# Kernel tuning notes

Measured on AMD Instinct MI355X. Metric: run time of the kernel, lower is better.

The kernel has to match this reference:

```python
import jax, jax.numpy as jnp
import numpy as np

B, C, H, W = 4, 128, 64, 64


def setup_inputs() -> dict:
    key = jax.random.key(0)
    k1, k2 = jax.random.split(key)
    x = jax.random.normal(k1, (B, C, H, W), dtype=jnp.float32)
    # 1x1 conv kv_mapper: weight [C_out, C_in], bias [C_out]; C_out == C_in == C
    W_kv = jax.random.normal(k2, (C, C), dtype=jnp.float32) * (1.0 / np.sqrt(C))
    b_kv = jnp.zeros((C,), dtype=jnp.float32)
    return {"x": x, "W_kv": W_kv, "b_kv": b_kv}


def reference(x, W_kv, b_kv):
    b, c, h, w = x.shape
    # kv_mapper: 1x1 conv  -> v: [b, c, h, w]
    v = jnp.einsum('bchw,oc->bohw', x, W_kv) + b_kv[None, :, None, None]
    # rearrange 'b c h w -> b (h w) c'
    L = h * w
    values = v.reshape(b, c, L).transpose(0, 2, 1)    # keys == values
    queries = x.reshape(b, c, L).transpose(0, 2, 1)
    # scaled dot-product attention, full [b, L, L] scores
    scores = jnp.einsum('blc,btc->blt', queries, values) / jnp.sqrt(jnp.asarray(c, x.dtype))
    attn = jax.nn.softmax(scores, axis=-1)
    out = jnp.einsum('blt,btv->blv', attn, values)    # [b, L, c]
    # rearrange 'b (h w) c -> b c h w'
    return out.transpose(0, 2, 1).reshape(b, c, h, w)
```

## Files before the change

kernel.cpp:

```cpp
#include <hip/hip_runtime.h>

#define LQ 4096
#define CH 128
#define NB 4
#define QSCALE 0.12753139626233174f
#define MAXCH 8
#define TILE_HW 8192

typedef __attribute__((ext_vector_type(8))) unsigned short ushort8;
typedef __attribute__((ext_vector_type(4))) unsigned short ushort4v;
typedef __attribute__((ext_vector_type(4))) unsigned int uint32x4;
typedef __attribute__((ext_vector_type(8))) __bf16 bf16x8;
typedef __attribute__((ext_vector_type(4))) float f32x4;

__device__ inline unsigned short f2bf(float f) {
    unsigned int u = __builtin_bit_cast(unsigned int, f);
    u += 0x7fffu + ((u >> 16) & 1u);
    return (unsigned short)(u >> 16);
}
__device__ inline float bf2f(unsigned short h) {
    unsigned int u = (unsigned int)h << 16;
    return __builtin_bit_cast(float, u);
}
__device__ inline unsigned int bfpack2(float a, float b) {
    unsigned int ua = __builtin_bit_cast(unsigned int, a) + 0x8000u;
    unsigned int ub = __builtin_bit_cast(unsigned int, b) + 0x8000u;
    return (ua >> 16) | (ub & 0xffff0000u);
}
__device__ inline void gload_lds16(const unsigned short* g, unsigned short* l) {
    __builtin_amdgcn_global_load_lds(
        (const __attribute__((address_space(1))) unsigned int*)(g),
        (__attribute__((address_space(3))) unsigned int*)(l), 16, 0, 0);
}

__global__ __launch_bounds__(256) void prep_kernel(
    const float* __restrict__ x, const float* __restrict__ Wkv,
    const float* __restrict__ bkv,
    unsigned short* __restrict__ Vt2, unsigned short* __restrict__ Vc2)
{
    __shared__ __align__(16) unsigned short xs[64 * 136];
    __shared__ __align__(16) unsigned short vs[128 * 72];
    const int tid = threadIdx.x;
    const int lane = tid & 63;
    const int wave = tid >> 6;
    const int quad = lane >> 4, l16 = lane & 15;
    const int b = blockIdx.x & 3;
    const int T = blockIdx.x >> 2;
    const int l0 = T << 6;

    {
        const f32x4* xg4 = (const f32x4*)(x + (size_t)b * CH * LQ + l0);
        #pragma unroll
        for (int i = 0; i < 8; ++i) {
            int idx = i * 256 + tid;
            int c = idx >> 4, l4 = idx & 15;
            f32x4 v = xg4[c * (LQ / 4) + l4];
            #pragma unroll
            for (int m = 0; m < 4; ++m) xs[(l4 * 4 + m) * 136 + c] = f2bf(v[m]);
        }
    }
    __syncthreads();

    const int wo = wave * 32;
    f32x4 acc[2][4];
    #pragma unroll
    for (int ot = 0; ot < 2; ++ot)
        #pragma unroll
        for (int lt = 0; lt < 4; ++lt) acc[ot][lt] = f32x4{0.f, 0.f, 0.f, 0.f};

    #pragma unroll
    for (int kc = 0; kc < 4; ++kc) {
        bf16x8 af[2];
        #pragma unroll
        for (int ot = 0; ot < 2; ++ot) {
            const float* wrow = Wkv + (size_t)(wo + ot * 16 + l16) * CH + kc * 32 + quad * 8;
            f32x4 w0 = *(const f32x4*)(wrow);
            f32x4 w1 = *(const f32x4*)(wrow + 4);
            ushort8 a;
            #pragma unroll
            for (int j = 0; j < 4; ++j) { a[j] = f2bf(w0[j]); a[j + 4] = f2bf(w1[j]); }
            af[ot] = __builtin_bit_cast(bf16x8, a);
        }
        #pragma unroll
        for (int lt = 0; lt < 4; ++lt) {
            bf16x8 bf = __builtin_bit_cast(bf16x8,
                *(const ushort8*)(xs + (lt * 16 + l16) * 136 + kc * 32 + quad * 8));
            #pragma unroll
            for (int ot = 0; ot < 2; ++ot)
                acc[ot][lt] = __builtin_amdgcn_mfma_f32_16x16x32_bf16(af[ot], bf, acc[ot][lt], 0, 0, 0);
        }
    }
    #pragma unroll
    for (int ot = 0; ot < 2; ++ot) {
        float bias[4];
        #pragma unroll
        for (int r = 0; r < 4; ++r) bias[r] = bkv[wo + ot * 16 + quad * 4 + r];
        #pragma unroll
        for (int lt = 0; lt < 4; ++lt)
            #pragma unroll
            for (int r = 0; r < 4; ++r)
                vs[(wo + ot * 16 + quad * 4 + r) * 72 + lt * 16 + l16] =
                    f2bf(acc[ot][lt][r] + bias[r]);
    }
    __syncthreads();
    const size_t tbase = ((size_t)b * 64 + T) * TILE_HW;
    #pragma unroll
    for (int i = 0; i < 4; ++i) {
        const int ci = i * 256 + tid;
        const int g = ci >> 6, ls = ci & 63;
        const int nt = g >> 2, kc = g & 3, qs = ls >> 4, l16s = ls & 15;
        ushort8 v;
        #pragma unroll
        for (int j = 0; j < 8; ++j) v[j] = vs[(kc * 32 + qs * 8 + j) * 72 + nt * 16 + l16s];
        *(ushort8*)(Vt2 + tbase + (size_t)ci * 8) = v;
    }
    #pragma unroll
    for (int i = 0; i < 4; ++i) {
        const int ci = i * 256 + tid;
        const int g = ci >> 6, ls = ci & 63;
        const int a = g >> 3, nc = g & 7, qs = ls >> 4, l16s = ls & 15;
        const int base = (nc * 16 + l16s) * 72 + a * 32 + qs * 4;
        ushort4v lo4 = *(const ushort4v*)(vs + base);
        ushort4v hi4 = *(const ushort4v*)(vs + base + 16);
        ushort8 v;
        #pragma unroll
        for (int j = 0; j < 4; ++j) { v[j] = lo4[j]; v[j + 4] = hi4[j]; }
        *(ushort8*)(Vc2 + tbase + (size_t)ci * 8) = v;
    }
}

__global__ __launch_bounds__(256, 2) void attn_kernel(
    const float* __restrict__ x, const unsigned short* __restrict__ Vt2,
    const unsigned short* __restrict__ Vc2,
    unsigned short* __restrict__ Opart, float* __restrict__ Lsum, int titers)
{
    __shared__ __align__(16) unsigned short bufA[TILE_HW];
    __shared__ __align__(16) unsigned short bufB[TILE_HW];
    const int tid = threadIdx.x;
    const int wave = tid >> 6, lane = tid & 63;
    const int quad = lane >> 4, l16 = lane & 15;
    const int b = blockIdx.x & 3;
    const int rest = blockIdx.x >> 2;
    const int qtile = rest & 31;
    const int chunk = rest >> 5;
    const int q0w = (qtile << 7) + (wave << 5);
    const int Tbase = chunk * titers;

    const unsigned short* vtb = Vt2 + (size_t)b * 64 * TILE_HW;
    const unsigned short* vcb = Vc2 + (size_t)b * 64 * TILE_HW;

    auto issueA = [&](int T) {
        const unsigned short* sa = vtb + (size_t)T * TILE_HW + lane * 8;
        #pragma unroll
        for (int g = 0; g < 4; ++g) {
            const int go = (wave * 4 + g) * 512;
            gload_lds16(sa + go, &bufA[go]);
        }
    };
    auto issueB = [&](int T) {
        const unsigned short* sb = vcb + (size_t)T * TILE_HW + lane * 8;
        #pragma unroll
        for (int g = 0; g < 4; ++g) {
            const int go = (wave * 4 + g) * 512;
            gload_lds16(sb + go, &bufB[go]);
        }
    };
    issueA(Tbase);

    bf16x8 qf[2][4];
    #pragma unroll
    for (int mt = 0; mt < 2; ++mt)
        #pragma unroll
        for (int kc = 0; kc < 4; ++kc) {
            ushort8 v;
            #pragma unroll
            for (int j = 0; j < 8; ++j) {
                int c = kc * 32 + quad * 8 + j;
                v[j] = f2bf(x[((size_t)b * CH + c) * LQ + q0w + mt * 16 + l16] * QSCALE);
            }
            qf[mt][kc] = __builtin_bit_cast(bf16x8, v);
        }

    f32x4 oacc[2][8];
    #pragma unroll
    for (int mt = 0; mt < 2; ++mt)
        #pragma unroll
        for (int i = 0; i < 8; ++i) oacc[mt][i] = f32x4{0.f, 0.f, 0.f, 0.f};
    float lsum[2] = {0.f, 0.f};

    for (int it = 0; it < titers; ++it) {
        asm volatile("s_waitcnt vmcnt(0)" ::: "memory");
        __builtin_amdgcn_s_barrier();
        issueB(Tbase + it);

        uint32x4 pk[2][2];

        #pragma unroll
        for (int nt = 0; nt < 4; ++nt) {
            const int aIdx = nt >> 1, h = nt & 1;
            bf16x8 vA[4];
            #pragma unroll
            for (int kc = 0; kc < 4; ++kc)
                vA[kc] = __builtin_bit_cast(bf16x8,
                    *(const ushort8*)(bufA + (nt * 4 + kc) * 512 + lane * 8));
            f32x4 s[2];
            __builtin_amdgcn_s_setprio(1);
            #pragma unroll
            for (int mt = 0; mt < 2; ++mt) {
                s[mt] = f32x4{0.f, 0.f, 0.f, 0.f};
                #pragma unroll
                for (int kc = 0; kc < 4; ++kc)
                    s[mt] = __builtin_amdgcn_mfma_f32_16x16x32_bf16(vA[kc], qf[mt][kc], s[mt], 0, 0, 0);
            }
            __builtin_amdgcn_s_setprio(0);
            #pragma unroll
            for (int mt = 0; mt < 2; ++mt) {
                float p0 = __builtin_amdgcn_exp2f(s[mt][0]);
                float p1 = __builtin_amdgcn_exp2f(s[mt][1]);
                float p2 = __builtin_amdgcn_exp2f(s[mt][2]);
                float p3 = __builtin_amdgcn_exp2f(s[mt][3]);
                lsum[mt] += (p0 + p1) + (p2 + p3);
                pk[mt][aIdx][h * 2 + 0] = bfpack2(p0, p1);
                pk[mt][aIdx][h * 2 + 1] = bfpack2(p2, p3);
            }
        }

        asm volatile("s_waitcnt vmcnt(0) lgkmcnt(0)" ::: "memory");
        __builtin_amdgcn_s_barrier();
        if (it + 1 < titers) issueA(Tbase + it + 1);

        __builtin_amdgcn_s_setprio(1);
        #pragma unroll
        for (int a = 0; a < 2; ++a) {
            bf16x8 pa0 = __builtin_bit_cast(bf16x8, pk[0][a]);
            bf16x8 pa1 = __builtin_bit_cast(bf16x8, pk[1][a]);
            #pragma unroll
            for (int nc = 0; nc < 8; ++nc) {
                bf16x8 vB = __builtin_bit_cast(bf16x8,
                    *(const ushort8*)(bufB + (a * 8 + nc) * 512 + lane * 8));
                oacc[0][nc] = __builtin_amdgcn_mfma_f32_16x16x32_bf16(pa0, vB, oacc[0][nc], 0, 0, 0);
                oacc[1][nc] = __builtin_amdgcn_mfma_f32_16x16x32_bf16(pa1, vB, oacc[1][nc], 0, 0, 0);
            }
        }
        __builtin_amdgcn_s_setprio(0);
    }
    const size_t pbase = ((size_t)(chunk * NB + b) * LQ);
    #pragma unroll
    for (int mt = 0; mt < 2; ++mt) {
        float v = lsum[mt];
        v += __shfl_xor(v, 16);
        v += __shfl_xor(v, 32);
        if (lane < 16) Lsum[pbase + q0w + mt * 16 + lane] = v;
    }
    #pragma unroll
    for (int mt = 0; mt < 2; ++mt)
        #pragma unroll
        for (int r = 0; r < 4; ++r) {
            const int q = q0w + mt * 16 + quad * 4 + r;
            unsigned short* orow = Opart + (pbase + q) * CH + l16;
            #pragma unroll
            for (int nc = 0; nc < 8; ++nc) orow[nc * 16] = f2bf(oacc[mt][nc][r]);
        }
}

__global__ __launch_bounds__(256) void combine_kernel(
    const unsigned short* __restrict__ Opart, const float* __restrict__ Lsum,
    float* __restrict__ out, int nchunk)
{
    __shared__ __align__(16) float ls[32 * 132];
    __shared__ float linv[32];
    const int tid = threadIdx.x;
    const int b = blockIdx.x & 3;
    const int q0 = (blockIdx.x >> 2) << 5;

    if (tid < 32) {
        float s = 0.f;
        for (int ch = 0; ch < nchunk; ++ch) s += Lsum[(size_t)(ch * NB + b) * LQ + q0 + tid];
        linv[tid] = 1.0f / s;
    }
    __syncthreads();
    {
        const int c8 = (tid & 15) * 8, qg = tid >> 4;
        #pragma unroll
        for (int i = 0; i < 2; ++i) {
            const int q = qg * 2 + i;
            float s[8];
            #pragma unroll
            for (int k = 0; k < 8; ++k) s[k] = 0.f;
            for (int ch = 0; ch < nchunk; ++ch) {
                ushort8 p = *(const ushort8*)(Opart +
                    ((size_t)(ch * NB + b) * LQ + q0 + q) * CH + c8);
                #pragma unroll
                for (int k = 0; k < 8; ++k) s[k] += bf2f(p[k]);
            }
            const float li = linv[q];
            f32x4 o0, o1;
            #pragma unroll
            for (int k = 0; k < 4; ++k) { o0[k] = s[k] * li; o1[k] = s[k + 4] * li; }
            *(f32x4*)(ls + q * 132 + c8) = o0;
            *(f32x4*)(ls + q * 132 + c8 + 4) = o1;
        }
    }
    __syncthreads();
    {
        const int c = tid & 127, qh = tid >> 7;
        float* dst = out + ((size_t)b * CH + c) * LQ + q0 + qh * 16;
        #pragma unroll
        for (int i = 0; i < 4; ++i) {
            f32x4 o;
            #pragma unroll
            for (int r = 0; r < 4; ++r) o[r] = ls[(qh * 16 + i * 4 + r) * 132 + c];
            ((f32x4*)dst)[i] = o;
        }
    }
}

extern "C" void kernel_launch(void* const* d_in, const int* in_sizes, int n_in,
                              void* d_out, int out_size, void* d_ws, size_t ws_size,
                              hipStream_t stream) {
    const float* x   = (const float*)d_in[0];
    const float* Wkv = (const float*)d_in[1];
    const float* bkv = (const float*)d_in[2];
    float* out = (float*)d_out;

    const size_t vElems = (size_t)NB * LQ * CH;
    unsigned short* Vt2 = (unsigned short*)d_ws;
    unsigned short* Vc2 = Vt2 + vElems;
    float* Lsum = (float*)(Vc2 + vElems);
    unsigned short* Opart = (unsigned short*)(Lsum + (size_t)MAXCH * NB * LQ);

    int nchunk = 4;
    const size_t fixed = 2 * vElems * 2 + (size_t)MAXCH * NB * LQ * 4;
    while (nchunk > 1 && fixed + (size_t)nchunk * NB * LQ * CH * 2 > ws_size) nchunk >>= 1;
    const int titers = (LQ / 64) / nchunk;

    prep_kernel<<<dim3(256), dim3(256), 0, stream>>>(x, Wkv, bkv, Vt2, Vc2);
    attn_kernel<<<dim3(128 * nchunk), dim3(256), 0, stream>>>(x, Vt2, Vc2, Opart, Lsum, titers);
    combine_kernel<<<dim3(512), dim3(256), 0, stream>>>(Opart, Lsum, out, nchunk);
}
```

Measured before the change: 116.6 us.

## Software-pipeline QK and PV stages with double-buffered V tile

Restructures the attention loop so the QK^T/exp of tile t is interleaved with the PV MMA of tile t-1, using ping-pong probability registers and a double-buffered bufB in LDS. The aim is to hide exp/VALU latency behind MFMA work and overlap global-to-LDS loads with compute across both stages. In exchange it uses more LDS (lower potential occupancy with 2 blocks/CU) and more registers. It also assumes titers is even (or handles the odd tail via a fixed prologue and epilogue), which could break for other chunk counts.

Result: no change. 118.2 us (+1.4%).

```diff
diff --git a/kernel.cpp b/kernel.cpp
--- a/kernel.cpp
+++ b/kernel.cpp
@@ -135,7 +135,7 @@
     unsigned short* __restrict__ Opart, float* __restrict__ Lsum, int titers)
 {
     __shared__ __align__(16) unsigned short bufA[TILE_HW];
-    __shared__ __align__(16) unsigned short bufB[TILE_HW];
+    __shared__ __align__(16) unsigned short bufB[2][TILE_HW];
     const int tid = threadIdx.x;
     const int wave = tid >> 6, lane = tid & 63;
     const int quad = lane >> 4, l16 = lane & 15;
@@ -157,12 +157,12 @@
             gload_lds16(sa + go, &bufA[go]);
         }
     };
-    auto issueB = [&](int T) {
+    auto issueB = [&](int T, int slot) {
         const unsigned short* sb = vcb + (size_t)T * TILE_HW + lane * 8;
         #pragma unroll
         for (int g = 0; g < 4; ++g) {
             const int go = (wave * 4 + g) * 512;
-            gload_lds16(sb + go, &bufB[go]);
+            gload_lds16(sb + go, &bufB[slot][go]);
         }
     };
     issueA(Tbase);
@@ -188,62 +188,96 @@
         for (int i = 0; i < 8; ++i) oacc[mt][i] = f32x4{0.f, 0.f, 0.f, 0.f};
     float lsum[2] = {0.f, 0.f};
 
-    for (int it = 0; it < titers; ++it) {
-        asm volatile("s_waitcnt vmcnt(0)" ::: "memory");
-        __builtin_amdgcn_s_barrier();
-        issueB(Tbase + it);
-
-        uint32x4 pk[2][2];
-
-        #pragma unroll
-        for (int nt = 0; nt < 4; ++nt) {
-            const int aIdx = nt >> 1, h = nt & 1;
-            bf16x8 vA[4];
-            #pragma unroll
-            for (int kc = 0; kc < 4; ++kc)
-                vA[kc] = __builtin_bit_cast(bf16x8,
-                    *(const ushort8*)(bufA + (nt * 4 + kc) * 512 + lane * 8));
-            f32x4 s[2];
-            __builtin_amdgcn_s_setprio(1);
-            #pragma unroll
-            for (int mt = 0; mt < 2; ++mt) {
-                s[mt] = f32x4{0.f, 0.f, 0.f, 0.f};
-                #pragma unroll
-                for (int kc = 0; kc < 4; ++kc)
-                    s[mt] = __builtin_amdgcn_mfma_f32_16x16x32_bf16(vA[kc], qf[mt][kc], s[mt], 0, 0, 0);
-            }
-            __builtin_amdgcn_s_setprio(0);
-            #pragma unroll
-            for (int mt = 0; mt < 2; ++mt) {
-                float p0 = __builtin_amdgcn_exp2f(s[mt][0]);
-                float p1 = __builtin_amdgcn_exp2f(s[mt][1]);
-                float p2 = __builtin_amdgcn_exp2f(s[mt][2]);
-                float p3 = __builtin_amdgcn_exp2f(s[mt][3]);
-                lsum[mt] += (p0 + p1) + (p2 + p3);
-                pk[mt][aIdx][h * 2 + 0] = bfpack2(p0, p1);
-                pk[mt][aIdx][h * 2 + 1] = bfpack2(p2, p3);
-            }
-        }
-
-        asm volatile("s_waitcnt vmcnt(0) lgkmcnt(0)" ::: "memory");
-        __builtin_amdgcn_s_barrier();
-        if (it + 1 < titers) issueA(Tbase + it + 1);
-
-        __builtin_amdgcn_s_setprio(1);
-        #pragma unroll
-        for (int a = 0; a < 2; ++a) {
-            bf16x8 pa0 = __builtin_bit_cast(bf16x8, pk[0][a]);
-            bf16x8 pa1 = __builtin_bit_cast(bf16x8, pk[1][a]);
-            #pragma unroll
-            for (int nc = 0; nc < 8; ++nc) {
-                bf16x8 vB = __builtin_bit_cast(bf16x8,
-                    *(const ushort8*)(bufB + (a * 8 + nc) * 512 + lane * 8));
-                oacc[0][nc] = __builtin_amdgcn_mfma_f32_16x16x32_bf16(pa0, vB, oacc[0][nc], 0, 0, 0);
-                oacc[1][nc] = __builtin_amdgcn_mfma_f32_16x16x32_bf16(pa1, vB, oacc[1][nc], 0, 0, 0);
-            }
-        }
-        __builtin_amdgcn_s_setprio(0);
-    }
+    uint32x4 pkE[2][2], pkO[2][2];
+
+#define QK_NT(nt, PK) { \
+    const int aIdx_ = (nt) >> 1, hh_ = (nt) & 1; \
+    bf16x8 vA_[4]; \
+    _Pragma("unroll") \
+    for (int kc = 0; kc < 4; ++kc) \
+        vA_[kc] = __builtin_bit_cast(bf16x8, \
+            *(const ushort8*)(bufA + ((nt) * 4 + kc) * 512 + lane * 8)); \
+    f32x4 s0_ = f32x4{0.f, 0.f, 0.f, 0.f}; \
+    f32x4 s1_ = f32x4{0.f, 0.f, 0.f, 0.f}; \
+    __builtin_amdgcn_s_setprio(1); \
+    _Pragma("unroll") \
+    for (int kc = 0; kc < 4; ++kc) { \
+        s0_ = __builtin_amdgcn_mfma_f32_16x16x32_bf16(vA_[kc], qf[0][kc], s0_, 0, 0, 0); \
+        s1_ = __builtin_amdgcn_mfma_f32_16x16x32_bf16(vA_[kc], qf[1][kc], s1_, 0, 0, 0); \
+    } \
+    __builtin_amdgcn_s_setprio(0); \
+    { \
+        float p0 = __builtin_amdgcn_exp2f(s0_[0]); \
+        float p1 = __builtin_amdgcn_exp2f(s0_[1]); \
+        float p2 = __builtin_amdgcn_exp2f(s0_[2]); \
+        float p3 = __builtin_amdgcn_exp2f(s0_[3]); \
+        lsum[0] += (p0 + p1) + (p2 + p3); \
+        PK[0][aIdx_][hh_ * 2 + 0] = bfpack2(p0, p1); \
+        PK[0][aIdx_][hh_ * 2 + 1] = bfpack2(p2, p3); \
+    } \
+    { \
+        float p0 = __builtin_amdgcn_exp2f(s1_[0]); \
+        float p1 = __builtin_amdgcn_exp2f(s1_[1]); \
+        float p2 = __builtin_amdgcn_exp2f(s1_[2]); \
+        float p3 = __builtin_amdgcn_exp2f(s1_[3]); \
+        lsum[1] += (p0 + p1) + (p2 + p3); \
+        PK[1][aIdx_][hh_ * 2 + 0] = bfpack2(p0, p1); \
+        PK[1][aIdx_][hh_ * 2 + 1] = bfpack2(p2, p3); \
+    } \
+}
+
+#define PV_PART(aa, nc0, PK, RS) { \
+    bf16x8 pa0_ = __builtin_bit_cast(bf16x8, PK[0][aa]); \
+    bf16x8 pa1_ = __builtin_bit_cast(bf16x8, PK[1][aa]); \
+    __builtin_amdgcn_s_setprio(1); \
+    _Pragma("unroll") \
+    for (int nc = (nc0); nc < (nc0) + 4; ++nc) { \
+        bf16x8 vB_ = __builtin_bit_cast(bf16x8, \
+            *(const ushort8*)(bufB[RS] + ((aa) * 8 + nc) * 512 + lane * 8)); \
+        oacc[0][nc] = __builtin_amdgcn_mfma_f32_16x16x32_bf16(pa0_, vB_, oacc[0][nc], 0, 0, 0); \
+        oacc[1][nc] = __builtin_amdgcn_mfma_f32_16x16x32_bf16(pa1_, vB_, oacc[1][nc], 0, 0, 0); \
+    } \
+    __builtin_amdgcn_s_setprio(0); \
+}
+
+#define MIXED_IT(itv, WS, PKW, PKR) \
+    issueB(Tbase + (itv), WS); \
+    asm volatile("s_waitcnt vmcnt(4)" ::: "memory"); \
+    __builtin_amdgcn_s_barrier(); \
+    QK_NT(0, PKW) PV_PART(0, 0, PKR, (WS) ^ 1) \
+    QK_NT(1, PKW) PV_PART(0, 4, PKR, (WS) ^ 1) \
+    QK_NT(2, PKW) PV_PART(1, 0, PKR, (WS) ^ 1) \
+    QK_NT(3, PKW) PV_PART(1, 4, PKR, (WS) ^ 1)
+
+#define END_IT(nextT) \
+    asm volatile("s_waitcnt lgkmcnt(0)" ::: "memory"); \
+    __builtin_amdgcn_s_barrier(); \
+    issueA(nextT);
+
+    issueB(Tbase, 0);
+    asm volatile("s_waitcnt vmcnt(4)" ::: "memory");
+    __builtin_amdgcn_s_barrier();
+    QK_NT(0, pkE) QK_NT(1, pkE) QK_NT(2, pkE) QK_NT(3, pkE)
+    END_IT(Tbase + 1)
+
+    for (int s = 1; s + 1 < titers; s += 2) {
+        MIXED_IT(s, 1, pkO, pkE)
+        END_IT(Tbase + s + 1)
+        MIXED_IT(s + 1, 0, pkE, pkO)
+        END_IT(Tbase + s + 2)
+    }
+
+    MIXED_IT(titers - 1, 1, pkO, pkE)
+    asm volatile("s_waitcnt vmcnt(0) lgkmcnt(0)" ::: "memory");
+    __builtin_amdgcn_s_barrier();
+    PV_PART(0, 0, pkO, 1) PV_PART(0, 4, pkO, 1)
+    PV_PART(1, 0, pkO, 1) PV_PART(1, 4, pkO, 1)
+
+#undef QK_NT
+#undef PV_PART
+#undef MIXED_IT
+#undef END_IT
+
     const size_t pbase = ((size_t)(chunk * NB + b) * LQ);
     #pragma unroll
     for (int mt = 0; mt < 2; ++mt) {
```

## Split key tile across two wave groups in 512-thread attention blocks

Applied to the files above, without the earlier changes.

The attention kernel doubles its block size to 8 waves. Each group of 4 waves processes half of every 64-key tile, computing both the scores and the PV products, and the two partial accumulators and row sums are reduced through shared memory at the end. This halves the per-wave MFMA work for each tile so more waves can hide latency on the same query tile. The costs are a 64KB LDS reduction buffer that likely limits residency to one block per CU, a tighter register cap that may cause spills, and duplicated Q fragment loads.

Result: slower. 125.5 us (+7.6%).

```diff
diff --git a/kernel.cpp b/kernel.cpp
--- a/kernel.cpp
+++ b/kernel.cpp
@@ -129,21 +129,24 @@
     }
 }
 
-__global__ __launch_bounds__(256, 2) void attn_kernel(
+__global__ __launch_bounds__(512, 2) void attn_kernel(
     const float* __restrict__ x, const unsigned short* __restrict__ Vt2,
     const unsigned short* __restrict__ Vc2,
     unsigned short* __restrict__ Opart, float* __restrict__ Lsum, int titers)
 {
     __shared__ __align__(16) unsigned short bufA[TILE_HW];
     __shared__ __align__(16) unsigned short bufB[TILE_HW];
+    __shared__ __align__(16) float red[16384];
+    __shared__ float lred[512];
     const int tid = threadIdx.x;
     const int wave = tid >> 6, lane = tid & 63;
     const int quad = lane >> 4, l16 = lane & 15;
+    const int qw = wave & 3, tw = wave >> 2;
     const int b = blockIdx.x & 3;
     const int rest = blockIdx.x >> 2;
     const int qtile = rest & 31;
     const int chunk = rest >> 5;
-    const int q0w = (qtile << 7) + (wave << 5);
+    const int q0w = (qtile << 7) + (qw << 5);
     const int Tbase = chunk * titers;
 
     const unsigned short* vtb = Vt2 + (size_t)b * 64 * TILE_HW;
@@ -152,16 +155,16 @@
     auto issueA = [&](int T) {
         const unsigned short* sa = vtb + (size_t)T * TILE_HW + lane * 8;
         #pragma unroll
-        for (int g = 0; g < 4; ++g) {
-            const int go = (wave * 4 + g) * 512;
+        for (int g = 0; g < 2; ++g) {
+            const int go = (wave * 2 + g) * 512;
             gload_lds16(sa + go, &bufA[go]);
         }
     };
     auto issueB = [&](int T) {
         const unsigned short* sb = vcb + (size_t)T * TILE_HW + lane * 8;
         #pragma unroll
-        for (int g = 0; g < 4; ++g) {
-            const int go = (wave * 4 + g) * 512;
+        for (int g = 0; g < 2; ++g) {
+            const int go = (wave * 2 + g) * 512;
             gload_lds16(sb + go, &bufB[go]);
         }
     };
@@ -193,11 +196,11 @@
         __builtin_amdgcn_s_barrier();
         issueB(Tbase + it);
 
-        uint32x4 pk[2][2];
-
-        #pragma unroll
-        for (int nt = 0; nt < 4; ++nt) {
-            const int aIdx = nt >> 1, h = nt & 1;
+        uint32x4 pk[2];
+
+        #pragma unroll
+        for (int h = 0; h < 2; ++h) {
+            const int nt = tw * 2 + h;
             bf16x8 vA[4];
             #pragma unroll
             for (int kc = 0; kc < 4; ++kc)
@@ -220,8 +223,8 @@
                 float p2 = __builtin_amdgcn_exp2f(s[mt][2]);
                 float p3 = __builtin_amdgcn_exp2f(s[mt][3]);
                 lsum[mt] += (p0 + p1) + (p2 + p3);
-                pk[mt][aIdx][h * 2 + 0] = bfpack2(p0, p1);
-                pk[mt][aIdx][h * 2 + 1] = bfpack2(p2, p3);
+                pk[mt][h * 2 + 0] = bfpack2(p0, p1);
+                pk[mt][h * 2 + 1] = bfpack2(p2, p3);
             }
         }
 
@@ -229,38 +232,55 @@
         __builtin_amdgcn_s_barrier();
         if (it + 1 < titers) issueA(Tbase + it + 1);
 
+        bf16x8 pa0 = __builtin_bit_cast(bf16x8, pk[0]);
+        bf16x8 pa1 = __builtin_bit_cast(bf16x8, pk[1]);
         __builtin_amdgcn_s_setprio(1);
         #pragma unroll
-        for (int a = 0; a < 2; ++a) {
-            bf16x8 pa0 = __builtin_bit_cast(bf16x8, pk[0][a]);
-            bf16x8 pa1 = __builtin_bit_cast(bf16x8, pk[1][a]);
-            #pragma unroll
-            for (int nc = 0; nc < 8; ++nc) {
-                bf16x8 vB = __builtin_bit_cast(bf16x8,
-                    *(const ushort8*)(bufB + (a * 8 + nc) * 512 + lane * 8));
-                oacc[0][nc] = __builtin_amdgcn_mfma_f32_16x16x32_bf16(pa0, vB, oacc[0][nc], 0, 0, 0);
-                oacc[1][nc] = __builtin_amdgcn_mfma_f32_16x16x32_bf16(pa1, vB, oacc[1][nc], 0, 0, 0);
-            }
+        for (int nc = 0; nc < 8; ++nc) {
+            bf16x8 vB = __builtin_bit_cast(bf16x8,
+                *(const ushort8*)(bufB + (tw * 8 + nc) * 512 + lane * 8));
+            oacc[0][nc] = __builtin_amdgcn_mfma_f32_16x16x32_bf16(pa0, vB, oacc[0][nc], 0, 0, 0);
+            oacc[1][nc] = __builtin_amdgcn_mfma_f32_16x16x32_bf16(pa1, vB, oacc[1][nc], 0, 0, 0);
         }
         __builtin_amdgcn_s_setprio(0);
     }
-    const size_t pbase = ((size_t)(chunk * NB + b) * LQ);
-    #pragma unroll
-    for (int mt = 0; mt < 2; ++mt) {
-        float v = lsum[mt];
-        v += __shfl_xor(v, 16);
-        v += __shfl_xor(v, 32);
-        if (lane < 16) Lsum[pbase + q0w + mt * 16 + lane] = v;
-    }
-    #pragma unroll
-    for (int mt = 0; mt < 2; ++mt)
-        #pragma unroll
-        for (int r = 0; r < 4; ++r) {
-            const int q = q0w + mt * 16 + quad * 4 + r;
-            unsigned short* orow = Opart + (pbase + q) * CH + l16;
-            #pragma unroll
-            for (int nc = 0; nc < 8; ++nc) orow[nc * 16] = f2bf(oacc[mt][nc][r]);
-        }
+
+    if (tw == 1) {
+        #pragma unroll
+        for (int mt = 0; mt < 2; ++mt) {
+            #pragma unroll
+            for (int nc = 0; nc < 8; ++nc)
+                *(f32x4*)(red + ((qw * 2 + mt) * 8 + nc) * 256 + lane * 4) = oacc[mt][nc];
+            lred[(qw * 2 + mt) * 64 + lane] = lsum[mt];
+        }
+    }
+    __syncthreads();
+    if (tw == 0) {
+        #pragma unroll
+        for (int mt = 0; mt < 2; ++mt) {
+            #pragma unroll
+            for (int nc = 0; nc < 8; ++nc)
+                oacc[mt][nc] += *(const f32x4*)(red + ((qw * 2 + mt) * 8 + nc) * 256 + lane * 4);
+            lsum[mt] += lred[(qw * 2 + mt) * 64 + lane];
+        }
+        const size_t pbase = ((size_t)(chunk * NB + b) * LQ);
+        #pragma unroll
+        for (int mt = 0; mt < 2; ++mt) {
+            float v = lsum[mt];
+            v += __shfl_xor(v, 16);
+            v += __shfl_xor(v, 32);
+            if (lane < 16) Lsum[pbase + q0w + mt * 16 + lane] = v;
+        }
+        #pragma unroll
+        for (int mt = 0; mt < 2; ++mt)
+            #pragma unroll
+            for (int r = 0; r < 4; ++r) {
+                const int q = q0w + mt * 16 + quad * 4 + r;
+                unsigned short* orow = Opart + (pbase + q) * CH + l16;
+                #pragma unroll
+                for (int nc = 0; nc < 8; ++nc) orow[nc * 16] = f2bf(oacc[mt][nc][r]);
+            }
+    }
 }
 
 __global__ __launch_bounds__(256) void combine_kernel(
@@ -335,6 +355,6 @@
     const int titers = (LQ / 64) / nchunk;
 
     prep_kernel<<<dim3(256), dim3(256), 0, stream>>>(x, Wkv, bkv, Vt2, Vc2);
-    attn_kernel<<<dim3(128 * nchunk), dim3(256), 0, stream>>>(x, Vt2, Vc2, Opart, Lsum, titers);
+    attn_kernel<<<dim3(128 * nchunk), dim3(512), 0, stream>>>(x, Vt2, Vc2, Opart, Lsum, titers);
     combine_kernel<<<dim3(512), dim3(256), 0, stream>>>(Opart, Lsum, out, nchunk);
 }
```

## Read K/V tiles directly from global memory instead of staging through LDS

Applied to the files above, without the earlier changes.

Removes the LDS double-buffer staging (global_load_lds into bufA/bufB) and the per-iteration barriers. Each wave now loads its K and V fragments straight from global memory (via L2/L1) into registers. This drops the synchronisation and LDS traffic, but all four waves in a block now fetch the same tile independently, and the loads are no longer prefetched ahead of use, which risks exposed memory latency.

New measurement: 177.9 us. +52.6%, slower.

```diff
diff --git a/kernel.cpp b/kernel.cpp
--- a/kernel.cpp
+++ b/kernel.cpp
@@ -26,11 +26,6 @@
     unsigned int ua = __builtin_bit_cast(unsigned int, a) + 0x8000u;
     unsigned int ub = __builtin_bit_cast(unsigned int, b) + 0x8000u;
     return (ua >> 16) | (ub & 0xffff0000u);
-}
-__device__ inline void gload_lds16(const unsigned short* g, unsigned short* l) {
-    __builtin_amdgcn_global_load_lds(
-        (const __attribute__((address_space(1))) unsigned int*)(g),
-        (__attribute__((address_space(3))) unsigned int*)(l), 16, 0, 0);
 }
 
 __global__ __launch_bounds__(256) void prep_kernel(
@@ -134,8 +129,6 @@
     const unsigned short* __restrict__ Vc2,
     unsigned short* __restrict__ Opart, float* __restrict__ Lsum, int titers)
 {
-    __shared__ __align__(16) unsigned short bufA[TILE_HW];
-    __shared__ __align__(16) unsigned short bufB[TILE_HW];
     const int tid = threadIdx.x;
     const int wave = tid >> 6, lane = tid & 63;
     const int quad = lane >> 4, l16 = lane & 15;
@@ -146,26 +139,8 @@
     const int q0w = (qtile << 7) + (wave << 5);
     const int Tbase = chunk * titers;
 
-    const unsigned short* vtb = Vt2 + (size_t)b * 64 * TILE_HW;
-    const unsigned short* vcb = Vc2 + (size_t)b * 64 * TILE_HW;
-
-    auto issueA = [&](int T) {
-        const unsigned short* sa = vtb + (size_t)T * TILE_HW + lane * 8;
-        #pragma unroll
-        for (int g = 0; g < 4; ++g) {
-            const int go = (wave * 4 + g) * 512;
-            gload_lds16(sa + go, &bufA[go]);
-        }
-    };
-    auto issueB = [&](int T) {
-        const unsigned short* sb = vcb + (size_t)T * TILE_HW + lane * 8;
-        #pragma unroll
-        for (int g = 0; g < 4; ++g) {
-            const int go = (wave * 4 + g) * 512;
-            gload_lds16(sb + go, &bufB[go]);
-        }
-    };
-    issueA(Tbase);
+    const unsigned short* vtb = Vt2 + (size_t)b * 64 * TILE_HW + (size_t)Tbase * TILE_HW + lane * 8;
+    const unsigned short* vcb = Vc2 + (size_t)b * 64 * TILE_HW + (size_t)Tbase * TILE_HW + lane * 8;
 
     bf16x8 qf[2][4];
     #pragma unroll
@@ -189,9 +164,8 @@
     float lsum[2] = {0.f, 0.f};
 
     for (int it = 0; it < titers; ++it) {
-        asm volatile("s_waitcnt vmcnt(0)" ::: "memory");
-        __builtin_amdgcn_s_barrier();
-        issueB(Tbase + it);
+        const unsigned short* tA = vtb + (size_t)it * TILE_HW;
+        const unsigned short* tB = vcb + (size_t)it * TILE_HW;
 
         uint32x4 pk[2][2];
 
@@ -202,7 +176,7 @@
             #pragma unroll
             for (int kc = 0; kc < 4; ++kc)
                 vA[kc] = __builtin_bit_cast(bf16x8,
-                    *(const ushort8*)(bufA + (nt * 4 + kc) * 512 + lane * 8));
+                    *(const ushort8*)(tA + (nt * 4 + kc) * 512));
             f32x4 s[2];
             __builtin_amdgcn_s_setprio(1);
             #pragma unroll
@@ -225,10 +199,6 @@
             }
         }
 
-        asm volatile("s_waitcnt vmcnt(0) lgkmcnt(0)" ::: "memory");
-        __builtin_amdgcn_s_barrier();
-        if (it + 1 < titers) issueA(Tbase + it + 1);
-
         __builtin_amdgcn_s_setprio(1);
         #pragma unroll
         for (int a = 0; a < 2; ++a) {
@@ -237,7 +207,7 @@
             #pragma unroll
             for (int nc = 0; nc < 8; ++nc) {
                 bf16x8 vB = __builtin_bit_cast(bf16x8,
-                    *(const ushort8*)(bufB + (a * 8 + nc) * 512 + lane * 8));
+                    *(const ushort8*)(tB + (a * 8 + nc) * 512));
                 oacc[0][nc] = __builtin_amdgcn_mfma_f32_16x16x32_bf16(pa0, vB, oacc[0][nc], 0, 0, 0);
                 oacc[1][nc] = __builtin_amdgcn_mfma_f32_16x16x32_bf16(pa1, vB, oacc[1][nc], 0, 0, 0);
             }
```
